# Kernel tuning notes

Hardware: AMD Instinct MI355X
Metric: run time of the kernel (lower is better)

## Reference

```python
import jax, jax.numpy as jnp
import numpy as np

P, T, L, K, N, K2, M, D = 16384, 8, 4096, 16, 2048, 32, 8, 64
ITER = 8
MM = {'flow_traffic': (0.0, 1e-4), 'flow_packets': (0.0, 1e-3), 'flow_packet_size': (0.0, 1e-3), 'link_capacity': (0.0, 1e-2)}


def _mlp2(x, w1, b1, w2, b2):
    return jax.nn.relu(jax.nn.relu(x @ w1 + b1) @ w2 + b2)


def _gru(x_proj, h, wh, bh):
    # Keras GRUCell, reset_after=True, gate order (z, r, h)
    hp = h @ wh + bh
    xz, xr, xc = jnp.split(x_proj, 3, axis=-1)
    hz, hr, hc = jnp.split(hp, 3, axis=-1)
    z = jax.nn.sigmoid(xz + hz)
    r = jax.nn.sigmoid(xr + hr)
    c = jnp.tanh(xc + r * hc)
    return z * h + (1.0 - z) * c


def setup_inputs() -> dict:
    key = jax.random.key(0)
    ks = iter(jax.random.split(key, 64))
    f32, i32 = jnp.float32, jnp.int32
    rn = lambda shape: jax.random.normal(next(ks), shape, dtype=f32) * 0.05
    inp = {}
    inp['flow_traffic'] = jax.random.uniform(next(ks), (P, 1), f32, 1.0, 1000.0)
    inp['flow_packets'] = jax.random.uniform(next(ks), (P, 1), f32, 1.0, 100.0)
    inp['flow_packet_size'] = jax.random.uniform(next(ks), (P, 1), f32, 64.0, 1500.0)
    inp['link_capacity'] = jax.random.uniform(next(ks), (L, 1), f32, 10.0, 100.0)
    inp['pe_w1'] = rn((3, D)); inp['pe_b1'] = jnp.zeros((D,), f32)
    inp['pe_w2'] = rn((D, D)); inp['pe_b2'] = jnp.zeros((D,), f32)
    inp['le_w1'] = rn((3, D)); inp['le_b1'] = jnp.zeros((D,), f32)
    inp['le_w2'] = rn((D, D)); inp['le_b2'] = jnp.zeros((D,), f32)
    inp['de_w1'] = rn((2, D)); inp['de_b1'] = jnp.zeros((D,), f32)
    inp['de_w2'] = rn((D, D)); inp['de_b2'] = jnp.zeros((D,), f32)
    for p in ('pgru', 'lgru', 'dgru'):
        inp[p + '_wx'] = rn((D, 3 * D)); inp[p + '_wh'] = rn((D, 3 * D))
        inp[p + '_bx'] = jnp.zeros((3 * D,), f32); inp[p + '_bh'] = jnp.zeros((3 * D,), f32)
    inp['ro_w1'] = rn((D, D // 2)); inp['ro_b1'] = jnp.zeros((D // 2,), f32)
    inp['ro_w2'] = rn((D // 2, D // 4)); inp['ro_b2'] = jnp.zeros((D // 4,), f32)
    inp['ro_w3'] = rn((D // 4, 1)); inp['ro_b3'] = jnp.zeros((1,), f32)
    inp['link_to_path'] = jax.random.randint(next(ks), (P, T), 0, L, i32)
    inp['node_to_path'] = jax.random.randint(next(ks), (P, T), 0, N, i32)
    inp['path_to_link'] = jnp.stack([jax.random.randint(next(ks), (L, K), 0, P, i32),
                                     jax.random.randint(next(ks), (L, K), 1, T + 1, i32)], axis=-1)
    inp['path_to_node'] = jnp.stack([jax.random.randint(next(ks), (N, K2), 0, P, i32),
                                     jax.random.randint(next(ks), (N, K2), 1, T + 1, i32)], axis=-1)
    inp['link_to_node'] = jax.random.randint(next(ks), (N, M), 0, L, i32)
    inp['nodes'] = jnp.zeros((N,), i32)
    inp['link_device_type'] = jnp.zeros((L,), i32)
    return inp


def reference(flow_traffic, flow_packets, flow_packet_size, link_capacity,
              pe_w1, pe_b1, pe_w2, pe_b2, le_w1, le_b1, le_w2, le_b2,
              de_w1, de_b1, de_w2, de_b2,
              pgru_wx, pgru_wh, pgru_bx, pgru_bh,
              lgru_wx, lgru_wh, lgru_bx, lgru_bh,
              dgru_wx, dgru_wh, dgru_bx, dgru_bh,
              ro_w1, ro_b1, ro_w2, ro_b2, ro_w3, ro_b3,
              link_to_path, node_to_path, path_to_link, path_to_node,
              link_to_node, nodes, link_device_type):
    # one_hot depth=1 -> 1.0 iff value==0
    ldt = (link_device_type == 0).astype(jnp.float32)[:, None]  # [L,1]
    # link load from path traffic
    load = flow_traffic[path_to_link[:, :, 0]].sum(axis=1) / (link_capacity * 1e9)  # [L,1]
    path_in = jnp.concatenate([
        (flow_traffic - MM['flow_traffic'][0]) * MM['flow_traffic'][1],
        (flow_packets - MM['flow_packets'][0]) * MM['flow_packets'][1],
        (flow_packet_size - MM['flow_packet_size'][0]) * MM['flow_packet_size'][1]], axis=1)
    path_state = _mlp2(path_in, pe_w1, pe_b1, pe_w2, pe_b2)  # [P,D]
    link_in = jnp.concatenate([(link_capacity - MM['link_capacity'][0]) * MM['link_capacity'][1], load, ldt], axis=1)
    link_state = _mlp2(link_in, le_w1, le_b1, le_w2, le_b2)  # [L,D]
    device_link_mean = link_state[link_to_node].sum(axis=1).mean(axis=1, keepdims=True)  # [N,1]
    devices_encoded = (nodes == 0).astype(jnp.float32)[:, None]  # [N,1]
    device_state = _mlp2(jnp.concatenate([devices_encoded, device_link_mean], axis=1),
                         de_w1, de_b1, de_w2, de_b2)  # [N,D]
    pl0, pl1 = path_to_link[:, :, 0], path_to_link[:, :, 1]
    pn0, pn1 = path_to_node[:, :, 0], path_to_node[:, :, 1]
    pss = None
    for _ in range(ITER):
        x = link_state[link_to_path] + device_state[node_to_path]  # [P,T,D]
        prev = path_state
        x_proj = jnp.swapaxes(x @ pgru_wx + pgru_bx, 0, 1)  # [T,P,3D]

        def step(h, xp):
            h2 = _gru(xp, h, pgru_wh, pgru_bh)
            return h2, h2

        path_state, seq = jax.lax.scan(step, path_state, x_proj)
        pss = jnp.concatenate([prev[:, None], jnp.swapaxes(seq, 0, 1)], axis=1)  # [P,T+1,D]
        link_state = _gru(pss[pl0, pl1].sum(axis=1) @ lgru_wx + lgru_bx, link_state, lgru_wh, lgru_bh)
        device_state = _gru(pss[pn0, pn1].sum(axis=1) @ dgru_wx + dgru_bx, device_state, dgru_wh, dgru_bh)
    h = jax.nn.relu(pss[:, 1:] @ ro_w1 + ro_b1)
    h = jax.nn.relu(h @ ro_w2 + ro_b2)
    occupancy = jax.nn.softplus(h @ ro_w3 + ro_b3)  # [P,T,1]
    delay = (occupancy / link_capacity[link_to_path]).sum(axis=1)  # [P,1]
    return delay
```

## Files before the change

kernel.cpp:

```cpp
#include <hip/hip_runtime.h>
#include <hip/hip_bf16.h>

static constexpr int PN = 16384;
static constexpr int TT = 8;
static constexpr int LN = 4096;
static constexpr int KG = 16;
static constexpr int NN = 2048;
static constexpr int K2G = 32;
static constexpr int MG = 8;
static constexpr int ITER = 8;

typedef __attribute__((ext_vector_type(8))) short short8b;
typedef __attribute__((ext_vector_type(4))) float f32x4;
typedef __attribute__((ext_vector_type(4))) unsigned int u32x4;

__device__ __forceinline__ float frcp(float x) {
    return __builtin_amdgcn_rcpf(x);
}
__device__ __forceinline__ float sigmoidf_(float x) {
    return frcp(1.0f + __expf(-x));
}
__device__ __forceinline__ float tanhf_(float x) {
    return 1.0f - 2.0f * frcp(__expf(2.0f * x) + 1.0f);
}
__device__ __forceinline__ float softplusf_(float x) {
    return fmaxf(x, 0.0f) + log1pf(__expf(-fabsf(x)));
}
__device__ __forceinline__ unsigned short f2bf(float f) {
    unsigned int x = __float_as_uint(f);
    unsigned int r = (x + 0x7fffu + ((x >> 16) & 1u)) >> 16;
    return (unsigned short)r;
}
__device__ __forceinline__ unsigned int pk2bf(float a, float b) {
    union { __hip_bfloat162 h; unsigned int u; } cvt;
    cvt.h = __float22bfloat162_rn(float2{a, b});
    return cvt.u;
}
__device__ __forceinline__ float bf2f(unsigned short u) {
    return __uint_as_float(((unsigned int)u) << 16);
}

__global__ __launch_bounds__(256) void k_setup(
    const float* __restrict__ ft, const float* __restrict__ fpk,
    const float* __restrict__ fps, const float* __restrict__ cap,
    const int* __restrict__ ptl, const int* __restrict__ ldt,
    const float* __restrict__ pe_w1, const float* __restrict__ pe_b1,
    const float* __restrict__ pe_w2, const float* __restrict__ pe_b2,
    const float* __restrict__ le_w1, const float* __restrict__ le_b1,
    const float* __restrict__ le_w2, const float* __restrict__ le_b2,
    const float* __restrict__ pgru_wx, const float* __restrict__ pgru_wh,
    const float* __restrict__ lgru_wx, const float* __restrict__ lgru_wh,
    const float* __restrict__ dgru_wx, const float* __restrict__ dgru_wh,
    unsigned short* __restrict__ pwxT, unsigned short* __restrict__ pwhT,
    unsigned short* __restrict__ lwxT, unsigned short* __restrict__ lwhT,
    unsigned short* __restrict__ dwxT, unsigned short* __restrict__ dwhT,
    float* __restrict__ path_state, float* __restrict__ link_state,
    unsigned short* __restrict__ lsb)
{
    int b = blockIdx.x;
    int tid = threadIdx.x;
    if (b >= 1280) {
        const float* srcs[6] = {pgru_wx, pgru_wh, lgru_wx, lgru_wh, dgru_wx, dgru_wh};
        unsigned short* dsts[6] = {pwxT, pwhT, lwxT, lwhT, dwxT, dwhT};
        int i = (b - 1280) * 256 + tid;
        int mi = i / 12288, o = i - mi * 12288;
        int n = o >> 6, k = o & 63;
        dsts[mi][o] = f2bf(srcs[mi][k * 192 + n]);
        return;
    }
    __shared__ __align__(16) float w2s[4096];
    __shared__ float w1s[192], b1s[64], b2s[64];
    __shared__ float h1s[4][64];
    bool isPath = (b < 1024);
    const float* w1p = isPath ? pe_w1 : le_w1;
    const float* b1p = isPath ? pe_b1 : le_b1;
    const float* w2p = isPath ? pe_w2 : le_w2;
    const float* b2p = isPath ? pe_b2 : le_b2;
    for (int i = tid; i < 4096; i += 256) w2s[i] = w2p[i];
    if (tid < 192) w1s[tid] = w1p[tid];
    if (tid < 64) { b1s[tid] = b1p[tid]; b2s[tid] = b2p[tid]; }
    __syncthreads();
    int rl = tid >> 6, d = tid & 63;
    int base = (isPath ? b : (b - 1024)) * 16;
    for (int rp = 0; rp < 4; ++rp) {
        int row = base + rp * 4 + rl;
        float h;
        if (isPath) {
            float x0 = ft[row]  * 1e-4f;
            float x1 = fpk[row] * 1e-3f;
            float x2 = fps[row] * 1e-3f;
            h = b1s[d] + x0 * w1s[d] + x1 * w1s[64 + d] + x2 * w1s[128 + d];
        } else {
            float v = 0.0f;
            if (d < 16) v = ft[ptl[(row * 16 + d) * 2]];
            v += __shfl_down(v, 8);
            v += __shfl_down(v, 4);
            v += __shfl_down(v, 2);
            v += __shfl_down(v, 1);
            float ssum = __shfl(v, 0);
            float cv = cap[row];
            float load = ssum * frcp(cv * 1e9f);
            float x2 = (ldt[row] == 0) ? 1.0f : 0.0f;
            h = b1s[d] + cv * 0.01f * w1s[d] + load * w1s[64 + d] + x2 * w1s[128 + d];
        }
        h1s[rl][d] = fmaxf(h, 0.0f);
        __syncthreads();
        float acc = b2s[d];
#pragma unroll 8
        for (int k = 0; k < 64; ++k) acc += h1s[rl][k] * w2s[k * 64 + d];
        float v = fmaxf(acc, 0.0f);
        if (isPath) {
            path_state[(size_t)row * 64 + d] = v;
        } else {
            link_state[(size_t)row * 64 + d] = v;
            lsb[(size_t)row * 64 + d] = f2bf(v);
        }
        __syncthreads();
    }
}

__global__ __launch_bounds__(256) void k_device_encode(
    const float* __restrict__ link_state, const int* __restrict__ ltn,
    const int* __restrict__ nodes,
    const float* __restrict__ w1, const float* __restrict__ b1,
    const float* __restrict__ w2, const float* __restrict__ b2,
    float* __restrict__ device_state, unsigned short* __restrict__ dsb)
{
    __shared__ __align__(16) float w2s[4096];
    __shared__ float h1s[4][64];
    int tid = threadIdx.x;
    for (int i = tid; i < 4096; i += 256) w2s[i] = w2[i];
    int rl = tid >> 6, d = tid & 63;
    int row = blockIdx.x * 4 + rl;
    float s = 0.0f;
#pragma unroll
    for (int m = 0; m < MG; ++m)
        s += link_state[(size_t)ltn[row * MG + m] * 64 + d];
#pragma unroll
    for (int o = 32; o > 0; o >>= 1) s += __shfl_xor(s, o);
    float dlm = s * (1.0f / 64.0f);
    float enc = (nodes[row] == 0) ? 1.0f : 0.0f;
    float h = b1[d] + enc * w1[d] + dlm * w1[64 + d];
    h1s[rl][d] = fmaxf(h, 0.0f);
    __syncthreads();
    float acc = b2[d];
#pragma unroll 8
    for (int k = 0; k < 64; ++k) acc += h1s[rl][k] * w2s[k * 64 + d];
    float v = fmaxf(acc, 0.0f);
    device_state[(size_t)row * 64 + d] = v;
    dsb[(size_t)row * 64 + d] = f2bf(v);
}

template <bool LAST>
__global__ __launch_bounds__(256, 4) void k_pscan(
    const unsigned short* __restrict__ lsb, const unsigned short* __restrict__ dsb,
    const int* __restrict__ ltp, const int* __restrict__ ntp,
    const unsigned short* __restrict__ wxT,
    const unsigned short* __restrict__ whT,
    const float* __restrict__ bx, const float* __restrict__ bh,
    float* __restrict__ path_state, unsigned short* __restrict__ pssb,
    const float* __restrict__ rw1, const float* __restrict__ rb1,
    const float* __restrict__ rw2, const float* __restrict__ rb2,
    const float* __restrict__ rw3, const float* __restrict__ rb3,
    const float* __restrict__ cap, float* __restrict__ out)
{
    __shared__ __align__(16) unsigned short Xs[8][16][72];
    __shared__ __align__(16) unsigned short Hb0[16][72];
    __shared__ int sIdx[256];
    __shared__ __align__(16) float rw1s[LAST ? 2048 : 4];
    __shared__ __align__(16) float rw2s[LAST ? 512 : 4];
    __shared__ float rw3s[16], rb1s[32], rb2s[16];
    int tid = threadIdx.x;
    int p0 = blockIdx.x * 16;

    if (LAST) {
        for (int i = tid; i < 2048; i += 256) rw1s[i] = rw1[i];
        for (int i = tid; i < 512; i += 256) rw2s[i] = rw2[i];
        if (tid < 16) rw3s[tid] = rw3[tid];
        if (tid < 32) rb1s[tid] = rb1[tid];
        if (tid < 16) rb2s[tid] = rb2[tid];
    }
    {
        int pi = tid >> 1;
        int m = pi & 15, t = pi >> 4;
        int gi = (p0 + m) * TT + t;
        sIdx[tid] = (tid & 1) ? __builtin_nontemporal_load(ntp + gi)
                              : __builtin_nontemporal_load(ltp + gi);
    }
    __syncthreads();
    {
        int j = tid & 15;
        int g = tid >> 4;
        uint2 A[8], B[8];
#pragma unroll
        for (int ro = 0; ro < 8; ++ro) {
            int pi = ro * 16 + g;
            int il = sIdx[pi * 2];
            int in = sIdx[pi * 2 + 1];
            A[ro] = *(const uint2*)(lsb + (size_t)il * 64 + j * 4);
            B[ro] = *(const uint2*)(dsb + (size_t)in * 64 + j * 4);
        }
#pragma unroll
        for (int ro = 0; ro < 8; ++ro) {
            float a0 = bf2f((unsigned short)A[ro].x);
            float a1 = bf2f((unsigned short)(A[ro].x >> 16));
            float a2 = bf2f((unsigned short)A[ro].y);
            float a3 = bf2f((unsigned short)(A[ro].y >> 16));
            float b0 = bf2f((unsigned short)B[ro].x);
            float b1 = bf2f((unsigned short)(B[ro].x >> 16));
            float b2 = bf2f((unsigned short)B[ro].y);
            float b3 = bf2f((unsigned short)(B[ro].y >> 16));
            uint2 u;
            u.x = pk2bf(a0 + b0, a1 + b1);
            u.y = pk2bf(a2 + b2, a3 + b3);
            *(uint2*)&Xs[ro][g][j * 4] = u;
        }
    }

    int lane = tid & 63, w = tid >> 6;
    int c = lane & 15, q = lane >> 4;
    int d = 16 * w + c;
    short8b fx[3][2], fh[3][2];
#pragma unroll
    for (int g = 0; g < 3; ++g)
#pragma unroll
        for (int kt = 0; kt < 2; ++kt) {
            int off = (g * 64 + 16 * w + c) * 64 + kt * 32 + q * 8;
            fx[g][kt] = *(const short8b*)(wxT + off);
            fh[g][kt] = *(const short8b*)(whT + off);
        }
    float bz = bx[d] + bh[d];
    float br = bx[64 + d] + bh[64 + d];
    float bxc = bx[128 + d];
    float bhc = bh[128 + d];
    float hold[4];
#pragma unroll
    for (int r_ = 0; r_ < 4; ++r_) {
        hold[r_] = path_state[(size_t)(p0 + q * 4 + r_) * 64 + d];
        Hb0[q * 4 + r_][d] = f2bf(hold[r_]);
    }
    __syncthreads();

    short8b aXc0 = *(const short8b*)&Xs[0][c][q * 8];
    short8b aXc1 = *(const short8b*)&Xs[0][c][32 + q * 8];

    for (int t = 0; t < TT; ++t) {
        f32x4 ax[3], ah[3];
        ax[0] = (f32x4){bz, bz, bz, bz};
        ax[1] = (f32x4){br, br, br, br};
        ax[2] = (f32x4){bxc, bxc, bxc, bxc};
        ah[0] = (f32x4){0.f, 0.f, 0.f, 0.f};
        ah[1] = (f32x4){0.f, 0.f, 0.f, 0.f};
        ah[2] = (f32x4){bhc, bhc, bhc, bhc};
        const unsigned short* hsrc = (t == 0) ? &Hb0[0][0] : &Xs[t - 1][0][0];
        short8b aH0 = *(const short8b*)(hsrc + c * 72 + q * 8);
        short8b aH1 = *(const short8b*)(hsrc + c * 72 + 32 + q * 8);
#pragma unroll
        for (int g = 0; g < 3; ++g) {
            ax[g] = __builtin_amdgcn_mfma_f32_16x16x32_bf16(aXc0, fx[g][0], ax[g], 0, 0, 0);
            ax[g] = __builtin_amdgcn_mfma_f32_16x16x32_bf16(aXc1, fx[g][1], ax[g], 0, 0, 0);
            ah[g] = __builtin_amdgcn_mfma_f32_16x16x32_bf16(aH0, fh[g][0], ah[g], 0, 0, 0);
            ah[g] = __builtin_amdgcn_mfma_f32_16x16x32_bf16(aH1, fh[g][1], ah[g], 0, 0, 0);
        }
        if (t < TT - 1) {
            aXc0 = *(const short8b*)&Xs[t + 1][c][q * 8];
            aXc1 = *(const short8b*)&Xs[t + 1][c][32 + q * 8];
        }
#pragma unroll
        for (int r_ = 0; r_ < 4; ++r_) {
            float z  = sigmoidf_(ax[0][r_] + ah[0][r_]);
            float rr = sigmoidf_(ax[1][r_] + ah[1][r_]);
            float cc = tanhf_(ax[2][r_] + rr * ah[2][r_]);
            float hn = cc + z * (hold[r_] - cc);
            hold[r_] = hn;
            Xs[t][q * 4 + r_][d] = f2bf(hn);
        }
        __syncthreads();
    }
    if (!LAST) {
#pragma unroll
        for (int r_ = 0; r_ < 4; ++r_)
            path_state[(size_t)(p0 + q * 4 + r_) * 64 + d] = hold[r_];
        {
            unsigned short* base = pssb + (size_t)p0 * TT * 64;
#pragma unroll
            for (int j = 0; j < 4; ++j) {
                int o = j * 2048 + tid * 8;
                int r = o >> 6;
                int c0 = o & 63;
                int m = r >> 3, t = r & 7;
                u32x4 v = *(const u32x4*)&Xs[t][m][c0];
                __builtin_nontemporal_store(v, (u32x4*)(base + o));
            }
        }
        return;
    }
    {
        int r = tid >> 1, hh = tid & 1;
        int m = r >> 3, t = r & 7;
        short8b rowv[8];
#pragma unroll
        for (int j = 0; j < 8; ++j)
            rowv[j] = *(const short8b*)&Xs[t][m][j * 8];
        float a1[16];
#pragma unroll
        for (int i = 0; i < 16; ++i) a1[i] = 0.f;
#pragma unroll 4
        for (int k = 0; k < 64; ++k) {
            float x = bf2f((unsigned short)rowv[k >> 3][k & 7]);
            const float* wr = &rw1s[k * 32 + hh * 16];
            float4 wa = *(const float4*)(wr);
            float4 wb = *(const float4*)(wr + 4);
            float4 wc = *(const float4*)(wr + 8);
            float4 wd = *(const float4*)(wr + 12);
            a1[0]  += x * wa.x; a1[1]  += x * wa.y; a1[2]  += x * wa.z; a1[3]  += x * wa.w;
            a1[4]  += x * wb.x; a1[5]  += x * wb.y; a1[6]  += x * wb.z; a1[7]  += x * wb.w;
            a1[8]  += x * wc.x; a1[9]  += x * wc.y; a1[10] += x * wc.z; a1[11] += x * wc.w;
            a1[12] += x * wd.x; a1[13] += x * wd.y; a1[14] += x * wd.z; a1[15] += x * wd.w;
        }
#pragma unroll
        for (int i = 0; i < 16; ++i)
            a1[i] = fmaxf(a1[i] + rb1s[hh * 16 + i], 0.0f);
        float h1[32];
#pragma unroll
        for (int i = 0; i < 16; ++i) {
            float o = __shfl_xor(a1[i], 1);
            h1[hh * 16 + i] = a1[i];
            h1[(1 - hh) * 16 + i] = o;
        }
        float a2[8];
#pragma unroll
        for (int i = 0; i < 8; ++i) a2[i] = 0.f;
#pragma unroll 4
        for (int k = 0; k < 32; ++k) {
            float x = h1[k];
            const float* wr = &rw2s[k * 16 + hh * 8];
            float4 wa = *(const float4*)(wr);
            float4 wb = *(const float4*)(wr + 4);
            a2[0] += x * wa.x; a2[1] += x * wa.y; a2[2] += x * wa.z; a2[3] += x * wa.w;
            a2[4] += x * wb.x; a2[5] += x * wb.y; a2[6] += x * wb.z; a2[7] += x * wb.w;
        }
#pragma unroll
        for (int i = 0; i < 8; ++i)
            a2[i] = fmaxf(a2[i] + rb2s[hh * 8 + i], 0.0f);
        float h2[16];
#pragma unroll
        for (int i = 0; i < 8; ++i) {
            float o = __shfl_xor(a2[i], 1);
            h2[hh * 8 + i] = a2[i];
            h2[(1 - hh) * 8 + i] = o;
        }
        float a3 = rb3[0];
#pragma unroll
        for (int k = 0; k < 16; ++k) a3 += h2[k] * rw3s[k];
        float occ = softplusf_(a3);
        float dcon = occ * frcp(cap[ltp[(p0 + m) * TT + t]]);
        float s = dcon;
        s += __shfl_xor(s, 2);
        s += __shfl_xor(s, 4);
        s += __shfl_xor(s, 8);
        if ((tid & 15) == 0) out[p0 + m] = s;
    }
}

template <int Kg>
__device__ __forceinline__ void edge_body(
    const unsigned short* __restrict__ wxT, const unsigned short* __restrict__ whT,
    const float* __restrict__ bx, const float* __restrict__ bh,
    const int* __restrict__ p2e, const unsigned short* __restrict__ pssb,
    float* __restrict__ state, unsigned short* __restrict__ smir, int blk)
{
    __shared__ int idxs[16 * Kg * 2];
    __shared__ __align__(16) unsigned short Ab[16][72];
    __shared__ __align__(16) unsigned short Hbs[16][72];
    __shared__ __align__(16) float Hf[16][68];
    int tid = threadIdx.x;
    int r0 = blk * 16;
    for (int i = tid; i < 16 * Kg * 2; i += 256)
        idxs[i] = p2e[(size_t)r0 * Kg * 2 + i];
    __syncthreads();
    {
        int r = tid >> 4, c4 = (tid & 15) * 4;
        int row = r0 + r;
        float4 s = {0.f, 0.f, 0.f, 0.f};
#pragma unroll
        for (int k = 0; k < Kg; ++k) {
            int pi = idxs[(r * Kg + k) * 2];
            int ti = idxs[(r * Kg + k) * 2 + 1];
            ushort4 v = *(const ushort4*)(pssb + ((size_t)pi * TT + ti - 1) * 64 + c4);
            s.x += bf2f(v.x); s.y += bf2f(v.y);
            s.z += bf2f(v.z); s.w += bf2f(v.w);
        }
        uint2 ua;
        ua.x = pk2bf(s.x, s.y); ua.y = pk2bf(s.z, s.w);
        *(uint2*)&Ab[r][c4] = ua;
        float4 hv = *(const float4*)(state + (size_t)row * 64 + c4);
        *(float4*)&Hf[r][c4] = hv;
        uint2 uh;
        uh.x = pk2bf(hv.x, hv.y); uh.y = pk2bf(hv.z, hv.w);
        *(uint2*)&Hbs[r][c4] = uh;
    }
    __syncthreads();
    int lane = tid & 63, w = tid >> 6;
    int c = lane & 15, q = lane >> 4;
    int d = 16 * w + c;
    short8b fx[3][2], fh[3][2];
#pragma unroll
    for (int g = 0; g < 3; ++g)
#pragma unroll
        for (int kt = 0; kt < 2; ++kt) {
            int off = (g * 64 + 16 * w + c) * 64 + kt * 32 + q * 8;
            fx[g][kt] = *(const short8b*)(wxT + off);
            fh[g][kt] = *(const short8b*)(whT + off);
        }
    float bz = bx[d] + bh[d];
    float br = bx[64 + d] + bh[64 + d];
    float bxc = bx[128 + d];
    float bhc = bh[128 + d];
    f32x4 ax[3], ah[3];
    ax[0] = (f32x4){bz, bz, bz, bz};
    ax[1] = (f32x4){br, br, br, br};
    ax[2] = (f32x4){bxc, bxc, bxc, bxc};
    ah[0] = (f32x4){0.f, 0.f, 0.f, 0.f};
    ah[1] = (f32x4){0.f, 0.f, 0.f, 0.f};
    ah[2] = (f32x4){bhc, bhc, bhc, bhc};
#pragma unroll
    for (int kt = 0; kt < 2; ++kt) {
        short8b aA = *(const short8b*)&Ab[c][kt * 32 + q * 8];
        short8b aH = *(const short8b*)&Hbs[c][kt * 32 + q * 8];
#pragma unroll
        for (int g = 0; g < 3; ++g) {
            ax[g] = __builtin_amdgcn_mfma_f32_16x16x32_bf16(aA, fx[g][kt], ax[g], 0, 0, 0);
            ah[g] = __builtin_amdgcn_mfma_f32_16x16x32_bf16(aH, fh[g][kt], ah[g], 0, 0, 0);
        }
    }
#pragma unroll
    for (int r = 0; r < 4; ++r) {
        int m = q * 4 + r;
        float z  = sigmoidf_(ax[0][r] + ah[0][r]);
        float rr = sigmoidf_(ax[1][r] + ah[1][r]);
        float cc = tanhf_(ax[2][r] + rr * ah[2][r]);
        float hn = cc + z * (Hf[m][d] - cc);
        state[(size_t)(r0 + m) * 64 + d] = hn;
        smir[(size_t)(r0 + m) * 64 + d] = f2bf(hn);
    }
}

__global__ __launch_bounds__(256) void k_edge_merged(
    const unsigned short* __restrict__ lwxT, const unsigned short* __restrict__ lwhT,
    const float* __restrict__ lbx, const float* __restrict__ lbh,
    const int* __restrict__ ptl,
    const unsigned short* __restrict__ dwxT, const unsigned short* __restrict__ dwhT,
    const float* __restrict__ dbx, const float* __restrict__ dbh,
    const int* __restrict__ ptn,
    const unsigned short* __restrict__ pssb,
    float* __restrict__ link_state, float* __restrict__ device_state,
    unsigned short* __restrict__ lsb, unsigned short* __restrict__ dsb)
{
    int b = blockIdx.x;
    if (b < LN / 16) {
        edge_body<KG>(lwxT, lwhT, lbx, lbh, ptl, pssb, link_state, lsb, b);
    } else {
        edge_body<K2G>(dwxT, dwhT, dbx, dbh, ptn, pssb, device_state, dsb, b - LN / 16);
    }
}

extern "C" void kernel_launch(void* const* d_in, const int* in_sizes, int n_in,
                              void* d_out, int out_size, void* d_ws, size_t ws_size,
                              hipStream_t stream) {
    const float* ft   = (const float*)d_in[0];
    const float* fpk  = (const float*)d_in[1];
    const float* fps  = (const float*)d_in[2];
    const float* cap  = (const float*)d_in[3];
    const float* pe_w1 = (const float*)d_in[4];
    const float* pe_b1 = (const float*)d_in[5];
    const float* pe_w2 = (const float*)d_in[6];
    const float* pe_b2 = (const float*)d_in[7];
    const float* le_w1 = (const float*)d_in[8];
    const float* le_b1 = (const float*)d_in[9];
    const float* le_w2 = (const float*)d_in[10];
    const float* le_b2 = (const float*)d_in[11];
    const float* de_w1 = (const float*)d_in[12];
    const float* de_b1 = (const float*)d_in[13];
    const float* de_w2 = (const float*)d_in[14];
    const float* de_b2 = (const float*)d_in[15];
    const float* pgru_wx = (const float*)d_in[16];
    const float* pgru_wh = (const float*)d_in[17];
    const float* pgru_bx = (const float*)d_in[18];
    const float* pgru_bh = (const float*)d_in[19];
    const float* lgru_wx = (const float*)d_in[20];
    const float* lgru_wh = (const float*)d_in[21];
    const float* lgru_bx = (const float*)d_in[22];
    const float* lgru_bh = (const float*)d_in[23];
    const float* dgru_wx = (const float*)d_in[24];
    const float* dgru_wh = (const float*)d_in[25];
    const float* dgru_bx = (const float*)d_in[26];
    const float* dgru_bh = (const float*)d_in[27];
    const float* ro_w1 = (const float*)d_in[28];
    const float* ro_b1 = (const float*)d_in[29];
    const float* ro_w2 = (const float*)d_in[30];
    const float* ro_b2 = (const float*)d_in[31];
    const float* ro_w3 = (const float*)d_in[32];
    const float* ro_b3 = (const float*)d_in[33];
    const int* ltp   = (const int*)d_in[34];
    const int* ntp   = (const int*)d_in[35];
    const int* ptl   = (const int*)d_in[36];
    const int* ptn   = (const int*)d_in[37];
    const int* ltn   = (const int*)d_in[38];
    const int* nodes = (const int*)d_in[39];
    const int* ldt   = (const int*)d_in[40];
    float* out = (float*)d_out;

    char* ws = (char*)d_ws;
    float* path_state = (float*)ws;      ws += (size_t)PN * 64 * 4;
    float* link_state = (float*)ws;      ws += (size_t)LN * 64 * 4;
    float* device_state = (float*)ws;    ws += (size_t)NN * 64 * 4;
    unsigned short* pssb = (unsigned short*)ws; ws += (size_t)PN * TT * 64 * 2;
    unsigned short* lsb  = (unsigned short*)ws; ws += (size_t)LN * 64 * 2;
    unsigned short* dsb  = (unsigned short*)ws; ws += (size_t)NN * 64 * 2;
    unsigned short* pwxT = (unsigned short*)ws; ws += 192 * 64 * 2;
    unsigned short* pwhT = (unsigned short*)ws; ws += 192 * 64 * 2;
    unsigned short* lwxT = (unsigned short*)ws; ws += 192 * 64 * 2;
    unsigned short* lwhT = (unsigned short*)ws; ws += 192 * 64 * 2;
    unsigned short* dwxT = (unsigned short*)ws; ws += 192 * 64 * 2;
    unsigned short* dwhT = (unsigned short*)ws; ws += 192 * 64 * 2;

    k_setup<<<1568, 256, 0, stream>>>(ft, fpk, fps, cap, ptl, ldt,
                                      pe_w1, pe_b1, pe_w2, pe_b2,
                                      le_w1, le_b1, le_w2, le_b2,
                                      pgru_wx, pgru_wh, lgru_wx, lgru_wh,
                                      dgru_wx, dgru_wh,
                                      pwxT, pwhT, lwxT, lwhT, dwxT, dwhT,
                                      path_state, link_state, lsb);
    k_device_encode<<<NN / 4, 256, 0, stream>>>(link_state, ltn, nodes, de_w1,
                                                de_b1, de_w2, de_b2, device_state, dsb);
    for (int it = 0; it < ITER - 1; ++it) {
        k_pscan<false><<<PN / 16, 256, 0, stream>>>(
            lsb, dsb, ltp, ntp, pwxT, pwhT, pgru_bx, pgru_bh,
            path_state, pssb, ro_w1, ro_b1, ro_w2, ro_b2, ro_w3, ro_b3, cap, out);
        k_edge_merged<<<LN / 16 + NN / 16, 256, 0, stream>>>(
            lwxT, lwhT, lgru_bx, lgru_bh, ptl,
            dwxT, dwhT, dgru_bx, dgru_bh, ptn,
            pssb, link_state, device_state, lsb, dsb);
    }
    k_pscan<true><<<PN / 16, 256, 0, stream>>>(
        lsb, dsb, ltp, ntp, pwxT, pwhT, pgru_bx, pgru_bh,
        path_state, pssb, ro_w1, ro_b1, ro_w2, ro_b2, ro_w3, ro_b3, cap, out);
}
```

Measured before the change: 388.9 us.

## Process two 16-path tiles per block in path-scan kernel

Each k_pscan block now handles 32 paths as two independent 16-row groups, interleaving their MFMA chains and GRU gate math within each timestep. This amortises the per-block load of the wx/wh weight fragments and the per-step barrier over twice as many paths, and gives the scheduler two independent dependency chains to hide MFMA latency. The cost is doubled LDS and register use, a launch bound relaxed to 2 waves per SIMD, and half as many blocks, which lowers occupancy and the number of blocks available to spread across CUs.

```diff
diff --git a/kernel.cpp b/kernel.cpp
--- a/kernel.cpp
+++ b/kernel.cpp
@@ -152,7 +152,7 @@
 }
 
 template <bool LAST>
-__global__ __launch_bounds__(256, 4) void k_pscan(
+__global__ __launch_bounds__(256, 2) void k_pscan(
     const unsigned short* __restrict__ lsb, const unsigned short* __restrict__ dsb,
     const int* __restrict__ ltp, const int* __restrict__ ntp,
     const unsigned short* __restrict__ wxT,
@@ -164,14 +164,14 @@
     const float* __restrict__ rw3, const float* __restrict__ rb3,
     const float* __restrict__ cap, float* __restrict__ out)
 {
-    __shared__ __align__(16) unsigned short Xs[8][16][72];
-    __shared__ __align__(16) unsigned short Hb0[16][72];
-    __shared__ int sIdx[256];
+    __shared__ __align__(16) unsigned short Xs[2][8][16][72];
+    __shared__ __align__(16) unsigned short Hb0[2][16][72];
+    __shared__ int sIdx[2][256];
     __shared__ __align__(16) float rw1s[LAST ? 2048 : 4];
     __shared__ __align__(16) float rw2s[LAST ? 512 : 4];
     __shared__ float rw3s[16], rb1s[32], rb2s[16];
     int tid = threadIdx.x;
-    int p0 = blockIdx.x * 16;
+    int p0 = blockIdx.x * 32;
 
     if (LAST) {
         for (int i = tid; i < 2048; i += 256) rw1s[i] = rw1[i];
@@ -180,40 +180,44 @@
         if (tid < 32) rb1s[tid] = rb1[tid];
         if (tid < 16) rb2s[tid] = rb2[tid];
     }
-    {
+#pragma unroll
+    for (int g2 = 0; g2 < 2; ++g2) {
         int pi = tid >> 1;
         int m = pi & 15, t = pi >> 4;
-        int gi = (p0 + m) * TT + t;
-        sIdx[tid] = (tid & 1) ? __builtin_nontemporal_load(ntp + gi)
-                              : __builtin_nontemporal_load(ltp + gi);
+        int gi = (p0 + g2 * 16 + m) * TT + t;
+        sIdx[g2][tid] = (tid & 1) ? __builtin_nontemporal_load(ntp + gi)
+                                  : __builtin_nontemporal_load(ltp + gi);
     }
     __syncthreads();
     {
         int j = tid & 15;
         int g = tid >> 4;
-        uint2 A[8], B[8];
-#pragma unroll
-        for (int ro = 0; ro < 8; ++ro) {
-            int pi = ro * 16 + g;
-            int il = sIdx[pi * 2];
-            int in = sIdx[pi * 2 + 1];
-            A[ro] = *(const uint2*)(lsb + (size_t)il * 64 + j * 4);
-            B[ro] = *(const uint2*)(dsb + (size_t)in * 64 + j * 4);
-        }
-#pragma unroll
-        for (int ro = 0; ro < 8; ++ro) {
-            float a0 = bf2f((unsigned short)A[ro].x);
-            float a1 = bf2f((unsigned short)(A[ro].x >> 16));
-            float a2 = bf2f((unsigned short)A[ro].y);
-            float a3 = bf2f((unsigned short)(A[ro].y >> 16));
-            float b0 = bf2f((unsigned short)B[ro].x);
-            float b1 = bf2f((unsigned short)(B[ro].x >> 16));
-            float b2 = bf2f((unsigned short)B[ro].y);
-            float b3 = bf2f((unsigned short)(B[ro].y >> 16));
-            uint2 u;
-            u.x = pk2bf(a0 + b0, a1 + b1);
-            u.y = pk2bf(a2 + b2, a3 + b3);
-            *(uint2*)&Xs[ro][g][j * 4] = u;
+#pragma unroll
+        for (int g2 = 0; g2 < 2; ++g2) {
+            uint2 A[8], B[8];
+#pragma unroll
+            for (int ro = 0; ro < 8; ++ro) {
+                int pi = ro * 16 + g;
+                int il = sIdx[g2][pi * 2];
+                int in = sIdx[g2][pi * 2 + 1];
+                A[ro] = *(const uint2*)(lsb + (size_t)il * 64 + j * 4);
+                B[ro] = *(const uint2*)(dsb + (size_t)in * 64 + j * 4);
+            }
+#pragma unroll
+            for (int ro = 0; ro < 8; ++ro) {
+                float a0 = bf2f((unsigned short)A[ro].x);
+                float a1 = bf2f((unsigned short)(A[ro].x >> 16));
+                float a2 = bf2f((unsigned short)A[ro].y);
+                float a3 = bf2f((unsigned short)(A[ro].y >> 16));
+                float b0 = bf2f((unsigned short)B[ro].x);
+                float b1 = bf2f((unsigned short)(B[ro].x >> 16));
+                float b2 = bf2f((unsigned short)B[ro].y);
+                float b3 = bf2f((unsigned short)(B[ro].y >> 16));
+                uint2 u;
+                u.x = pk2bf(a0 + b0, a1 + b1);
+                u.y = pk2bf(a2 + b2, a3 + b3);
+                *(uint2*)&Xs[g2][ro][g][j * 4] = u;
+            }
         }
     }
 
@@ -233,63 +237,85 @@
     float br = bx[64 + d] + bh[64 + d];
     float bxc = bx[128 + d];
     float bhc = bh[128 + d];
-    float hold[4];
+    float holdA[4], holdB[4];
 #pragma unroll
     for (int r_ = 0; r_ < 4; ++r_) {
-        hold[r_] = path_state[(size_t)(p0 + q * 4 + r_) * 64 + d];
-        Hb0[q * 4 + r_][d] = f2bf(hold[r_]);
+        holdA[r_] = path_state[(size_t)(p0 + q * 4 + r_) * 64 + d];
+        Hb0[0][q * 4 + r_][d] = f2bf(holdA[r_]);
+        holdB[r_] = path_state[(size_t)(p0 + 16 + q * 4 + r_) * 64 + d];
+        Hb0[1][q * 4 + r_][d] = f2bf(holdB[r_]);
     }
     __syncthreads();
 
-    short8b aXc0 = *(const short8b*)&Xs[0][c][q * 8];
-    short8b aXc1 = *(const short8b*)&Xs[0][c][32 + q * 8];
+    short8b aXA0 = *(const short8b*)&Xs[0][0][c][q * 8];
+    short8b aXA1 = *(const short8b*)&Xs[0][0][c][32 + q * 8];
+    short8b aXB0 = *(const short8b*)&Xs[1][0][c][q * 8];
+    short8b aXB1 = *(const short8b*)&Xs[1][0][c][32 + q * 8];
 
     for (int t = 0; t < TT; ++t) {
-        f32x4 ax[3], ah[3];
-        ax[0] = (f32x4){bz, bz, bz, bz};
-        ax[1] = (f32x4){br, br, br, br};
-        ax[2] = (f32x4){bxc, bxc, bxc, bxc};
-        ah[0] = (f32x4){0.f, 0.f, 0.f, 0.f};
-        ah[1] = (f32x4){0.f, 0.f, 0.f, 0.f};
-        ah[2] = (f32x4){bhc, bhc, bhc, bhc};
-        const unsigned short* hsrc = (t == 0) ? &Hb0[0][0] : &Xs[t - 1][0][0];
-        short8b aH0 = *(const short8b*)(hsrc + c * 72 + q * 8);
-        short8b aH1 = *(const short8b*)(hsrc + c * 72 + 32 + q * 8);
+        f32x4 axA[3], ahA[3], axB[3], ahB[3];
+        axA[0] = (f32x4){bz, bz, bz, bz};   axB[0] = axA[0];
+        axA[1] = (f32x4){br, br, br, br};   axB[1] = axA[1];
+        axA[2] = (f32x4){bxc, bxc, bxc, bxc}; axB[2] = axA[2];
+        ahA[0] = (f32x4){0.f, 0.f, 0.f, 0.f}; ahB[0] = ahA[0];
+        ahA[1] = (f32x4){0.f, 0.f, 0.f, 0.f}; ahB[1] = ahA[1];
+        ahA[2] = (f32x4){bhc, bhc, bhc, bhc}; ahB[2] = ahA[2];
+        const unsigned short* hA = (t == 0) ? &Hb0[0][0][0] : &Xs[0][t - 1][0][0];
+        const unsigned short* hB = (t == 0) ? &Hb0[1][0][0] : &Xs[1][t - 1][0][0];
+        short8b aHA0 = *(const short8b*)(hA + c * 72 + q * 8);
+        short8b aHA1 = *(const short8b*)(hA + c * 72 + 32 + q * 8);
+        short8b aHB0 = *(const short8b*)(hB + c * 72 + q * 8);
+        short8b aHB1 = *(const short8b*)(hB + c * 72 + 32 + q * 8);
 #pragma unroll
         for (int g = 0; g < 3; ++g) {
-            ax[g] = __builtin_amdgcn_mfma_f32_16x16x32_bf16(aXc0, fx[g][0], ax[g], 0, 0, 0);
-            ax[g] = __builtin_amdgcn_mfma_f32_16x16x32_bf16(aXc1, fx[g][1], ax[g], 0, 0, 0);
-            ah[g] = __builtin_amdgcn_mfma_f32_16x16x32_bf16(aH0, fh[g][0], ah[g], 0, 0, 0);
-            ah[g] = __builtin_amdgcn_mfma_f32_16x16x32_bf16(aH1, fh[g][1], ah[g], 0, 0, 0);
+            axA[g] = __builtin_amdgcn_mfma_f32_16x16x32_bf16(aXA0, fx[g][0], axA[g], 0, 0, 0);
+            axB[g] = __builtin_amdgcn_mfma_f32_16x16x32_bf16(aXB0, fx[g][0], axB[g], 0, 0, 0);
+            axA[g] = __builtin_amdgcn_mfma_f32_16x16x32_bf16(aXA1, fx[g][1], axA[g], 0, 0, 0);
+            axB[g] = __builtin_amdgcn_mfma_f32_16x16x32_bf16(aXB1, fx[g][1], axB[g], 0, 0, 0);
+            ahA[g] = __builtin_amdgcn_mfma_f32_16x16x32_bf16(aHA0, fh[g][0], ahA[g], 0, 0, 0);
+            ahB[g] = __builtin_amdgcn_mfma_f32_16x16x32_bf16(aHB0, fh[g][0], ahB[g], 0, 0, 0);
+            ahA[g] = __builtin_amdgcn_mfma_f32_16x16x32_bf16(aHA1, fh[g][1], ahA[g], 0, 0, 0);
+            ahB[g] = __builtin_amdgcn_mfma_f32_16x16x32_bf16(aHB1, fh[g][1], ahB[g], 0, 0, 0);
         }
         if (t < TT - 1) {
-            aXc0 = *(const short8b*)&Xs[t + 1][c][q * 8];
-            aXc1 = *(const short8b*)&Xs[t + 1][c][32 + q * 8];
+            aXA0 = *(const short8b*)&Xs[0][t + 1][c][q * 8];
+            aXA1 = *(const short8b*)&Xs[0][t + 1][c][32 + q * 8];
+            aXB0 = *(const short8b*)&Xs[1][t + 1][c][q * 8];
+            aXB1 = *(const short8b*)&Xs[1][t + 1][c][32 + q * 8];
         }
 #pragma unroll
         for (int r_ = 0; r_ < 4; ++r_) {
-            float z  = sigmoidf_(ax[0][r_] + ah[0][r_]);
-            float rr = sigmoidf_(ax[1][r_] + ah[1][r_]);
-            float cc = tanhf_(ax[2][r_] + rr * ah[2][r_]);
-            float hn = cc + z * (hold[r_] - cc);
-            hold[r_] = hn;
-            Xs[t][q * 4 + r_][d] = f2bf(hn);
+            float zA  = sigmoidf_(axA[0][r_] + ahA[0][r_]);
+            float rrA = sigmoidf_(axA[1][r_] + ahA[1][r_]);
+            float ccA = tanhf_(axA[2][r_] + rrA * ahA[2][r_]);
+            float hnA = ccA + zA * (holdA[r_] - ccA);
+            holdA[r_] = hnA;
+            Xs[0][t][q * 4 + r_][d] = f2bf(hnA);
+            float zB  = sigmoidf_(axB[0][r_] + ahB[0][r_]);
+            float rrB = sigmoidf_(axB[1][r_] + ahB[1][r_]);
+            float ccB = tanhf_(axB[2][r_] + rrB * ahB[2][r_]);
+            float hnB = ccB + zB * (holdB[r_] - ccB);
+            holdB[r_] = hnB;
+            Xs[1][t][q * 4 + r_][d] = f2bf(hnB);
         }
         __syncthreads();
     }
     if (!LAST) {
 #pragma unroll
-        for (int r_ = 0; r_ < 4; ++r_)
-            path_state[(size_t)(p0 + q * 4 + r_) * 64 + d] = hold[r_];
+        for (int r_ = 0; r_ < 4; ++r_) {
+            path_state[(size_t)(p0 + q * 4 + r_) * 64 + d] = holdA[r_];
+            path_state[(size_t)(p0 + 16 + q * 4 + r_) * 64 + d] = holdB[r_];
+        }
         {
             unsigned short* base = pssb + (size_t)p0 * TT * 64;
 #pragma unroll
-            for (int j = 0; j < 4; ++j) {
-                int o = j * 2048 + tid * 8;
+            for (int jj = 0; jj < 8; ++jj) {
+                int o = jj * 2048 + tid * 8;
                 int r = o >> 6;
                 int c0 = o & 63;
                 int m = r >> 3, t = r & 7;
-                u32x4 v = *(const u32x4*)&Xs[t][m][c0];
+                int g2 = m >> 4, ml = m & 15;
+                u32x4 v = *(const u32x4*)&Xs[g2][t][ml][c0];
                 __builtin_nontemporal_store(v, (u32x4*)(base + o));
             }
         }
@@ -298,68 +324,71 @@
     {
         int r = tid >> 1, hh = tid & 1;
         int m = r >> 3, t = r & 7;
-        short8b rowv[8];
-#pragma unroll
-        for (int j = 0; j < 8; ++j)
-            rowv[j] = *(const short8b*)&Xs[t][m][j * 8];
-        float a1[16];
-#pragma unroll
-        for (int i = 0; i < 16; ++i) a1[i] = 0.f;
+#pragma unroll
+        for (int g2 = 0; g2 < 2; ++g2) {
+            short8b rowv[8];
+#pragma unroll
+            for (int j = 0; j < 8; ++j)
+                rowv[j] = *(const short8b*)&Xs[g2][t][m][j * 8];
+            float a1[16];
+#pragma unroll
+            for (int i = 0; i < 16; ++i) a1[i] = 0.f;
 #pragma unroll 4
-        for (int k = 0; k < 64; ++k) {
-            float x = bf2f((unsigned short)rowv[k >> 3][k & 7]);
-            const float* wr = &rw1s[k * 32 + hh * 16];
-            float4 wa = *(const float4*)(wr);
-            float4 wb = *(const float4*)(wr + 4);
-            float4 wc = *(const float4*)(wr + 8);
-            float4 wd = *(const float4*)(wr + 12);
-            a1[0]  += x * wa.x; a1[1]  += x * wa.y; a1[2]  += x * wa.z; a1[3]  += x * wa.w;
-            a1[4]  += x * wb.x; a1[5]  += x * wb.y; a1[6]  += x * wb.z; a1[7]  += x * wb.w;
-            a1[8]  += x * wc.x; a1[9]  += x * wc.y; a1[10] += x * wc.z; a1[11] += x * wc.w;
-            a1[12] += x * wd.x; a1[13] += x * wd.y; a1[14] += x * wd.z; a1[15] += x * wd.w;
-        }
-#pragma unroll
-        for (int i = 0; i < 16; ++i)
-            a1[i] = fmaxf(a1[i] + rb1s[hh * 16 + i], 0.0f);
-        float h1[32];
-#pragma unroll
-        for (int i = 0; i < 16; ++i) {
-            float o = __shfl_xor(a1[i], 1);
-            h1[hh * 16 + i] = a1[i];
-            h1[(1 - hh) * 16 + i] = o;
-        }
-        float a2[8];
-#pragma unroll
-        for (int i = 0; i < 8; ++i) a2[i] = 0.f;
+            for (int k = 0; k < 64; ++k) {
+                float x = bf2f((unsigned short)rowv[k >> 3][k & 7]);
+                const float* wr = &rw1s[k * 32 + hh * 16];
+                float4 wa = *(const float4*)(wr);
+                float4 wb = *(const float4*)(wr + 4);
+                float4 wc = *(const float4*)(wr + 8);
+                float4 wd = *(const float4*)(wr + 12);
+                a1[0]  += x * wa.x; a1[1]  += x * wa.y; a1[2]  += x * wa.z; a1[3]  += x * wa.w;
+                a1[4]  += x * wb.x; a1[5]  += x * wb.y; a1[6]  += x * wb.z; a1[7]  += x * wb.w;
+                a1[8]  += x * wc.x; a1[9]  += x * wc.y; a1[10] += x * wc.z; a1[11] += x * wc.w;
+                a1[12] += x * wd.x; a1[13] += x * wd.y; a1[14] += x * wd.z; a1[15] += x * wd.w;
+            }
+#pragma unroll
+            for (int i = 0; i < 16; ++i)
+                a1[i] = fmaxf(a1[i] + rb1s[hh * 16 + i], 0.0f);
+            float h1[32];
+#pragma unroll
+            for (int i = 0; i < 16; ++i) {
+                float o = __shfl_xor(a1[i], 1);
+                h1[hh * 16 + i] = a1[i];
+                h1[(1 - hh) * 16 + i] = o;
+            }
+            float a2[8];
+#pragma unroll
+            for (int i = 0; i < 8; ++i) a2[i] = 0.f;
 #pragma unroll 4
-        for (int k = 0; k < 32; ++k) {
-            float x = h1[k];
-            const float* wr = &rw2s[k * 16 + hh * 8];
-            float4 wa = *(const float4*)(wr);
-            float4 wb = *(const float4*)(wr + 4);
-            a2[0] += x * wa.x; a2[1] += x * wa.y; a2[2] += x * wa.z; a2[3] += x * wa.w;
-            a2[4] += x * wb.x; a2[5] += x * wb.y; a2[6] += x * wb.z; a2[7] += x * wb.w;
-        }
-#pragma unroll
-        for (int i = 0; i < 8; ++i)
-            a2[i] = fmaxf(a2[i] + rb2s[hh * 8 + i], 0.0f);
-        float h2[16];
-#pragma unroll
-        for (int i = 0; i < 8; ++i) {
-            float o = __shfl_xor(a2[i], 1);
-            h2[hh * 8 + i] = a2[i];
-            h2[(1 - hh) * 8 + i] = o;
-        }
-        float a3 = rb3[0];
-#pragma unroll
-        for (int k = 0; k < 16; ++k) a3 += h2[k] * rw3s[k];
-        float occ = softplusf_(a3);
-        float dcon = occ * frcp(cap[ltp[(p0 + m) * TT + t]]);
-        float s = dcon;
-        s += __shfl_xor(s, 2);
-        s += __shfl_xor(s, 4);
-        s += __shfl_xor(s, 8);
-        if ((tid & 15) == 0) out[p0 + m] = s;
+            for (int k = 0; k < 32; ++k) {
+                float x = h1[k];
+                const float* wr = &rw2s[k * 16 + hh * 8];
+                float4 wa = *(const float4*)(wr);
+                float4 wb = *(const float4*)(wr + 4);
+                a2[0] += x * wa.x; a2[1] += x * wa.y; a2[2] += x * wa.z; a2[3] += x * wa.w;
+                a2[4] += x * wb.x; a2[5] += x * wb.y; a2[6] += x * wb.z; a2[7] += x * wb.w;
+            }
+#pragma unroll
+            for (int i = 0; i < 8; ++i)
+                a2[i] = fmaxf(a2[i] + rb2s[hh * 8 + i], 0.0f);
+            float h2[16];
+#pragma unroll
+            for (int i = 0; i < 8; ++i) {
+                float o = __shfl_xor(a2[i], 1);
+                h2[hh * 8 + i] = a2[i];
+                h2[(1 - hh) * 8 + i] = o;
+            }
+            float a3 = rb3[0];
+#pragma unroll
+            for (int k = 0; k < 16; ++k) a3 += h2[k] * rw3s[k];
+            float occ = softplusf_(a3);
+            float dcon = occ * frcp(cap[ltp[(p0 + g2 * 16 + m) * TT + t]]);
+            float s = dcon;
+            s += __shfl_xor(s, 2);
+            s += __shfl_xor(s, 4);
+            s += __shfl_xor(s, 8);
+            if ((tid & 15) == 0) out[p0 + g2 * 16 + m] = s;
+        }
     }
 }
 
@@ -535,7 +564,7 @@
     k_device_encode<<<NN / 4, 256, 0, stream>>>(link_state, ltn, nodes, de_w1,
                                                 de_b1, de_w2, de_b2, device_state, dsb);
     for (int it = 0; it < ITER - 1; ++it) {
-        k_pscan<false><<<PN / 16, 256, 0, stream>>>(
+        k_pscan<false><<<PN / 32, 256, 0, stream>>>(
             lsb, dsb, ltp, ntp, pwxT, pwhT, pgru_bx, pgru_bh,
             path_state, pssb, ro_w1, ro_b1, ro_w2, ro_b2, ro_w3, ro_b3, cap, out);
         k_edge_merged<<<LN / 16 + NN / 16, 256, 0, stream>>>(
@@ -543,7 +572,7 @@
             dwxT, dwhT, dgru_bx, dgru_bh, ptn,
             pssb, link_state, device_state, lsb, dsb);
     }
-    k_pscan<true><<<PN / 16, 256, 0, stream>>>(
+    k_pscan<true><<<PN / 32, 256, 0, stream>>>(
         lsb, dsb, ltp, ntp, pwxT, pwhT, pgru_bx, pgru_bh,
         path_state, pssb, ro_w1, ro_b1, ro_w2, ro_b2, ro_w3, ro_b3, cap, out);
 }
```

Measured after the change: 415.0 us. 1.07x slower.
